# Optimization experiments

Measured on AMD Instinct MI355X. Metric: run time of the kernel, lower is better.

The kernel has to match this reference:

```python
import jax, jax.numpy as jnp
import numpy as np

B, S, F_IN, F_OUT, K = 4, 4096, 64, 64, 32


def setup_inputs() -> dict:
    key = jax.random.key(0)
    k1, k2, k3 = jax.random.split(key, 3)
    X = jax.random.normal(k1, (B, S, F_IN), dtype=jnp.float32)
    M = jax.random.normal(k2, (B, S, K), dtype=jnp.float32)
    # xavier_uniform for weight: bound = sqrt(6/(fan_in+fan_out))
    bound = float(np.sqrt(6.0 / (F_IN + F_OUT)))
    weight = jax.random.uniform(k3, (F_IN, F_OUT), dtype=jnp.float32,
                                minval=-bound, maxval=bound)
    bias = jnp.zeros((F_OUT,), dtype=jnp.float32)
    return {"X": X, "M": M, "weight": weight, "bias": bias}


def reference(X, M, weight, bias):
    # similarity = softmax(relu(M M^T), axis=-1)  -> [B, S, S]
    sim_raw = jnp.einsum('bsk,btk->bst', M, M)
    sim = jax.nn.softmax(jax.nn.relu(sim_raw), axis=-1)
    # X W  -> [B, S, F_OUT]
    Xw = jnp.einsum('bsf,fo->bso', X, weight)
    # mode='add': (I + A) Xw = Xw + A @ Xw  (identity matmul folded)
    Z = Xw + jnp.einsum('bst,bto->bso', sim, Xw)
    Z = Z + bias
    # dropout is identity at inference (eval mode)
    return Z
```

## Files before the change

kernel.cpp:

```cpp
#include <hip/hip_runtime.h>
#include <cstdint>

#define BATCH  4
#define SLEN   4096
#define FDIM   64
#define KDIM   32
#define KSPLIT 8
#define CHUNK  (SLEN / KSPLIT)

typedef __attribute__((ext_vector_type(8))) short bf16x8;
typedef __attribute__((ext_vector_type(4))) float f32x4;

static __device__ __forceinline__ short f2bf(float f) {
    union { float f; unsigned u; } v; v.f = f;
    unsigned r = v.u + 0x7fffu + ((v.u >> 16) & 1u);
    return (short)(r >> 16);
}
static __device__ __forceinline__ float bf2f(short s) {
    union { unsigned u; float f; } v;
    v.u = ((unsigned)(unsigned short)s) << 16;
    return v.f;
}
static __device__ __forceinline__ unsigned pack2bf(float a, float b) {
    union { float f; unsigned u; } x, y; x.f = a; y.f = b;
    unsigned ra = x.u + 0x7fffu + ((x.u >> 16) & 1u);
    unsigned rb = y.u + 0x7fffu + ((y.u >> 16) & 1u);
    return __builtin_amdgcn_perm(rb, ra, 0x07060302u);
}

__global__ __launch_bounds__(256) void prep(const float4* __restrict__ M4,
                                            ushort4* __restrict__ H4,
                                            ushort4* __restrict__ L4,
                                            const float* __restrict__ X,
                                            const float4* __restrict__ W4,
                                            float4* __restrict__ V4,
                                            short* __restrict__ Vt) {
    const int blk = blockIdx.y * gridDim.x + blockIdx.x;
#pragma unroll
    for (int r = 0; r < 2; ++r) {
        int i = (blk * 2 + r) * 256 + threadIdx.x;
        float4 m = M4[i];
        ushort4 h, l;
        h.x = (unsigned short)f2bf(m.x); l.x = (unsigned short)f2bf(m.x - bf2f((short)h.x));
        h.y = (unsigned short)f2bf(m.y); l.y = (unsigned short)f2bf(m.y - bf2f((short)h.y));
        h.z = (unsigned short)f2bf(m.z); l.z = (unsigned short)f2bf(m.z - bf2f((short)h.z));
        h.w = (unsigned short)f2bf(m.w); l.w = (unsigned short)f2bf(m.w - bf2f((short)h.w));
        H4[i] = h; L4[i] = l;
    }
    __shared__ float t[64][65];
    const int b  = blockIdx.y;
    const int s0 = blockIdx.x * 64;
    const int o4 = threadIdx.x & 15;
    const int rq = threadIdx.x >> 4;
#pragma unroll
    for (int half = 0; half < 4; ++half) {
        int r = half * 16 + rq;
        const float* __restrict__ xr = X + ((size_t)b * SLEN + s0 + r) * FDIM;
        float4 acc = make_float4(0.f, 0.f, 0.f, 0.f);
#pragma unroll
        for (int f = 0; f < FDIM; ++f) {
            float4 w = W4[f * 16 + o4];
            float  x = xr[f];
            acc.x = fmaf(x, w.x, acc.x);
            acc.y = fmaf(x, w.y, acc.y);
            acc.z = fmaf(x, w.z, acc.z);
            acc.w = fmaf(x, w.w, acc.w);
        }
        V4[((size_t)b * SLEN + s0 + r) * 16 + o4] = acc;
        t[r][o4 * 4 + 0] = acc.x;
        t[r][o4 * 4 + 1] = acc.y;
        t[r][o4 * 4 + 2] = acc.z;
        t[r][o4 * 4 + 3] = acc.w;
    }
    __syncthreads();
    const int c0 = threadIdx.x & 63;
    const int r0 = threadIdx.x >> 6;
    const int pc = (c0 & 32) | (((c0 >> 2) & 3) << 3) | (((c0 >> 4) & 1) << 2)
                 | (c0 & 3);
#pragma unroll
    for (int i = 0; i < 16; ++i) {
        int f = r0 + i * 4;
        Vt[((size_t)b * FDIM + f) * SLEN + s0 + pc] = f2bf(t[c0][f]);
    }
}

__global__ __launch_bounds__(256) void attn_mfma(const short* __restrict__ Mhi,
                                                 const short* __restrict__ Mlo,
                                                 const short* __restrict__ Vt,
                                                 float* __restrict__ accP,
                                                 float* __restrict__ lP) {
    const int bid  = blockIdx.x;
    const int slab = (bid & 7) + 8 * (bid >> 8);
    const int qblk = (bid >> 3) & 31;
    const int b    = slab >> 3;
    const int ks   = slab & 7;

    const int tid  = threadIdx.x;
    const int wave = tid >> 6;
    const int lane = tid & 63;
    const int col  = lane & 15;
    const int quad = lane >> 4;
    const int qbase = qblk * 128 + wave * 32;
    const int k0    = ks * CHUNK;

    const short* __restrict__ Mbh = Mhi + (size_t)b * SLEN * KDIM;
    const short* __restrict__ Mbl = Mlo + (size_t)b * SLEN * KDIM;
    const short* __restrict__ Vb  = Vt  + (size_t)b * FDIM * SLEN;

    __shared__ short khi[2][64 * 40];
    __shared__ short klo[2][64 * 40];
    __shared__ short vsh[2][2][64 * 40];

    bf16x8 Qh[2], Ql[2];
#pragma unroll
    for (int tq = 0; tq < 2; ++tq) {
        int qo = (qbase + tq * 16 + col) * KDIM + quad * 8;
        Qh[tq] = *(const bf16x8*)(Mbh + qo);
        Ql[tq] = *(const bf16x8*)(Mbl + qo);
    }

    f32x4 accf[2][4];
#pragma unroll
    for (int tq = 0; tq < 2; ++tq)
#pragma unroll
        for (int fg = 0; fg < 4; ++fg) accf[tq][fg] = (f32x4){0.f, 0.f, 0.f, 0.f};
    float lacc[2] = {0.f, 0.f};

    const int srow  = tid >> 2;
    const int spart = tid & 3;

    {
        bf16x8 rkh = *(const bf16x8*)(Mbh + (k0 + srow) * KDIM + spart * 8);
        bf16x8 rkl = *(const bf16x8*)(Mbl + (k0 + srow) * KDIM + spart * 8);
        bf16x8 rv0 = *(const bf16x8*)(Vb + (size_t)srow * SLEN + k0 + spart * 8);
        bf16x8 rv1 = *(const bf16x8*)(Vb + (size_t)srow * SLEN + k0 + 32 + spart * 8);
        *(bf16x8*)(khi[0]    + srow * 40 + spart * 8) = rkh;
        *(bf16x8*)(klo[0]    + srow * 40 + spart * 8) = rkl;
        *(bf16x8*)(vsh[0][0] + srow * 40 + spart * 8) = rv0;
        *(bf16x8*)(vsh[0][1] + srow * 40 + spart * 8) = rv1;
    }
    __syncthreads();

    int p = 0;
#pragma unroll 1
    for (int kt = k0; kt < k0 + CHUNK; kt += 64) {
        const int ktn  = kt + 64;
        const bool more = ktn < k0 + CHUNK;
        bf16x8 nkh, nkl, nv0, nv1;
        if (more) {
            nkh = *(const bf16x8*)(Mbh + (ktn + srow) * KDIM + spart * 8);
            nkl = *(const bf16x8*)(Mbl + (ktn + srow) * KDIM + spart * 8);
            nv0 = *(const bf16x8*)(Vb + (size_t)srow * SLEN + ktn + spart * 8);
            nv1 = *(const bf16x8*)(Vb + (size_t)srow * SLEN + ktn + 32 + spart * 8);
        }

        const short* __restrict__ KH = khi[p];
        const short* __restrict__ KL = klo[p];
        bf16x8 Kh[4], Kl[4];
#pragma unroll
        for (int t = 0; t < 4; ++t) {
            Kh[t] = *(const bf16x8*)(KH + (t * 16 + col) * 40 + quad * 8);
            Kl[t] = *(const bf16x8*)(KL + (t * 16 + col) * 40 + quad * 8);
        }
        bf16x8 Vv[4][2];
#pragma unroll
        for (int fg = 0; fg < 4; ++fg)
#pragma unroll
            for (int h = 0; h < 2; ++h)
                Vv[fg][h] = *(const bf16x8*)(vsh[p][h]
                                             + (fg * 16 + col) * 40 + quad * 8);

#pragma unroll
        for (int tq = 0; tq < 2; ++tq) {
            f32x4 z = (f32x4){0.f, 0.f, 0.f, 0.f};
            f32x4 c[4];
#pragma unroll
            for (int t = 0; t < 4; ++t) {
                c[t] = __builtin_amdgcn_mfma_f32_16x16x32_bf16(Kh[t], Ql[tq], z, 0, 0, 0);
                c[t] = __builtin_amdgcn_mfma_f32_16x16x32_bf16(Kl[t], Qh[tq], c[t], 0, 0, 0);
                c[t] = __builtin_amdgcn_mfma_f32_16x16x32_bf16(Kh[t], Qh[tq], c[t], 0, 0, 0);
            }
#pragma unroll
            for (int g = 0; g < 2; ++g) {
                float e0 = __expf(fmaxf(c[2 * g][0], 0.f));
                float e1 = __expf(fmaxf(c[2 * g][1], 0.f));
                float e2 = __expf(fmaxf(c[2 * g][2], 0.f));
                float e3 = __expf(fmaxf(c[2 * g][3], 0.f));
                float e4 = __expf(fmaxf(c[2 * g + 1][0], 0.f));
                float e5 = __expf(fmaxf(c[2 * g + 1][1], 0.f));
                float e6 = __expf(fmaxf(c[2 * g + 1][2], 0.f));
                float e7 = __expf(fmaxf(c[2 * g + 1][3], 0.f));
                lacc[tq] += ((e0 + e1) + (e2 + e3)) + ((e4 + e5) + (e6 + e7));

                union { unsigned u[4]; bf16x8 v; } pa;
                pa.u[0] = pack2bf(e0, e1);
                pa.u[1] = pack2bf(e2, e3);
                pa.u[2] = pack2bf(e4, e5);
                pa.u[3] = pack2bf(e6, e7);
#pragma unroll
                for (int fg = 0; fg < 4; ++fg)
                    accf[tq][fg] = __builtin_amdgcn_mfma_f32_16x16x32_bf16(
                        pa.v, Vv[fg][g], accf[tq][fg], 0, 0, 0);
            }
        }

        if (more) {
            *(bf16x8*)(khi[p ^ 1]    + srow * 40 + spart * 8) = nkh;
            *(bf16x8*)(klo[p ^ 1]    + srow * 40 + spart * 8) = nkl;
            *(bf16x8*)(vsh[p ^ 1][0] + srow * 40 + spart * 8) = nv0;
            *(bf16x8*)(vsh[p ^ 1][1] + srow * 40 + spart * 8) = nv1;
        }
        __syncthreads();
        p ^= 1;
    }

#pragma unroll
    for (int tq = 0; tq < 2; ++tq) {
#pragma unroll
        for (int j = 0; j < 4; ++j) {
            int q = qbase + tq * 16 + quad * 4 + j;
            size_t base = ((size_t)b * SLEN + q) * KSPLIT + ks;
            float* __restrict__ op = accP + base * FDIM;
#pragma unroll
            for (int fg = 0; fg < 4; ++fg)
                op[fg * 16 + col] = accf[tq][fg][j];
        }
        float lv = lacc[tq];
        lv += __shfl_xor(lv, 16);
        lv += __shfl_xor(lv, 32);
        if (quad == 0) {
            int q = qbase + tq * 16 + col;
            lP[((size_t)b * SLEN + q) * KSPLIT + ks] = lv;
        }
    }
}

__global__ __launch_bounds__(256) void combine_kernel(const float4* __restrict__ V4,
                                                      const float4* __restrict__ accP4,
                                                      const float* __restrict__ lP,
                                                      const float4* __restrict__ bias4,
                                                      float4* __restrict__ out4) {
    int i  = blockIdx.x * 256 + threadIdx.x;
    int o4 = i & 15;
    int row = i >> 4;
    float nx = 0.f, ny = 0.f, nz = 0.f, nw = 0.f, den = 0.f;
#pragma unroll
    for (int k = 0; k < KSPLIT; ++k) {
        float4 a = accP4[((size_t)row * KSPLIT + k) * 16 + o4];
        nx += a.x; ny += a.y; nz += a.z; nw += a.w;
        den += lP[(size_t)row * KSPLIT + k];
    }
    float r = 1.f / den;
    float4 v = V4[i];
    float4 bb = bias4[o4];
    float4 o;
    o.x = v.x + nx * r + bb.x;
    o.y = v.y + ny * r + bb.y;
    o.z = v.z + nz * r + bb.z;
    o.w = v.w + nw * r + bb.w;
    out4[i] = o;
}

extern "C" void kernel_launch(void* const* d_in, const int* in_sizes, int n_in,
                              void* d_out, int out_size, void* d_ws, size_t ws_size,
                              hipStream_t stream) {
    const float* X    = (const float*)d_in[0];
    const float* M    = (const float*)d_in[1];
    const float* W    = (const float*)d_in[2];
    const float* bias = (const float*)d_in[3];
    float* out = (float*)d_out;

    const size_t vElems = (size_t)BATCH * SLEN * FDIM;
    const size_t mElems = (size_t)BATCH * SLEN * KDIM;
    const size_t rows   = (size_t)BATCH * SLEN;

    float* Vf   = (float*)d_ws;
    float* accP = Vf + vElems;
    float* lP   = accP + vElems * KSPLIT;
    short* Mhi  = (short*)(lP + rows * KSPLIT);
    short* Mlo  = Mhi + mElems;
    short* Vt   = Mlo + mElems;

    prep<<<dim3(SLEN / 64, BATCH), 256, 0, stream>>>(
        (const float4*)M, (ushort4*)Mhi, (ushort4*)Mlo,
        X, (const float4*)W, (float4*)Vf, Vt);

    attn_mfma<<<dim3((SLEN / 128) * BATCH * KSPLIT), 256, 0, stream>>>(
        Mhi, Mlo, Vt, accP, lP);

    combine_kernel<<<(int)(vElems / 1024), 256, 0, stream>>>(
        (const float4*)Vf, (const float4*)accP, lP, (const float4*)bias,
        (float4*)out);
}
```

Baseline: 124.2 us.

## Double queries per wave, pre-scale Q by log2e, and drop LDS double buffering

Each wave now handles 64 queries instead of 32, so every K/V tile staged in LDS is reused across twice as many query rows, and the grid is halved. The query copy of M is pre-multiplied by log2(e) in the prep kernel, so the softmax exponent can use the native exp2 instead of __expf. The PV product is reordered so each V fragment is read from LDS once and applied to all four query tiles. LDS double buffering is replaced by a single buffer with two barriers per tile, with occupancy set through launch_bounds(256,2). This trades fewer blocks, more registers and the loss of load/compute overlap for better reuse and cheaper exponentials.

```diff
diff --git a/kernel.cpp b/kernel.cpp
--- a/kernel.cpp
+++ b/kernel.cpp
@@ -31,21 +31,29 @@
 __global__ __launch_bounds__(256) void prep(const float4* __restrict__ M4,
                                             ushort4* __restrict__ H4,
                                             ushort4* __restrict__ L4,
+                                            ushort4* __restrict__ QH4,
+                                            ushort4* __restrict__ QL4,
                                             const float* __restrict__ X,
                                             const float4* __restrict__ W4,
                                             float4* __restrict__ V4,
                                             short* __restrict__ Vt) {
     const int blk = blockIdx.y * gridDim.x + blockIdx.x;
+    const float LOG2E = 1.4426950408889634f;
 #pragma unroll
     for (int r = 0; r < 2; ++r) {
         int i = (blk * 2 + r) * 256 + threadIdx.x;
         float4 m = M4[i];
-        ushort4 h, l;
+        ushort4 h, l, sh, sl;
         h.x = (unsigned short)f2bf(m.x); l.x = (unsigned short)f2bf(m.x - bf2f((short)h.x));
         h.y = (unsigned short)f2bf(m.y); l.y = (unsigned short)f2bf(m.y - bf2f((short)h.y));
         h.z = (unsigned short)f2bf(m.z); l.z = (unsigned short)f2bf(m.z - bf2f((short)h.z));
         h.w = (unsigned short)f2bf(m.w); l.w = (unsigned short)f2bf(m.w - bf2f((short)h.w));
-        H4[i] = h; L4[i] = l;
+        float sx = m.x * LOG2E, sy = m.y * LOG2E, sz = m.z * LOG2E, sw = m.w * LOG2E;
+        sh.x = (unsigned short)f2bf(sx); sl.x = (unsigned short)f2bf(sx - bf2f((short)sh.x));
+        sh.y = (unsigned short)f2bf(sy); sl.y = (unsigned short)f2bf(sy - bf2f((short)sh.y));
+        sh.z = (unsigned short)f2bf(sz); sl.z = (unsigned short)f2bf(sz - bf2f((short)sh.z));
+        sh.w = (unsigned short)f2bf(sw); sl.w = (unsigned short)f2bf(sw - bf2f((short)sh.w));
+        H4[i] = h; L4[i] = l; QH4[i] = sh; QL4[i] = sl;
     }
     __shared__ float t[64][65];
     const int b  = blockIdx.y;
@@ -84,94 +92,79 @@
     }
 }
 
-__global__ __launch_bounds__(256) void attn_mfma(const short* __restrict__ Mhi,
-                                                 const short* __restrict__ Mlo,
-                                                 const short* __restrict__ Vt,
-                                                 float* __restrict__ accP,
-                                                 float* __restrict__ lP) {
+__global__ __launch_bounds__(256, 2) void attn_mfma(const short* __restrict__ Mhi,
+                                                    const short* __restrict__ Mlo,
+                                                    const short* __restrict__ Qhi,
+                                                    const short* __restrict__ Qlo,
+                                                    const short* __restrict__ Vt,
+                                                    float* __restrict__ accP,
+                                                    float* __restrict__ lP) {
     const int bid  = blockIdx.x;
-    const int slab = (bid & 7) + 8 * (bid >> 8);
-    const int qblk = (bid >> 3) & 31;
-    const int b    = slab >> 3;
-    const int ks   = slab & 7;
+    const int xcd  = bid & 7;
+    const int slot = bid >> 3;
+    const int g    = xcd + 8 * (slot >> 4);
+    const int qblk = slot & 15;
+    const int b    = g >> 3;
+    const int ks   = g & 7;
 
     const int tid  = threadIdx.x;
     const int wave = tid >> 6;
     const int lane = tid & 63;
     const int col  = lane & 15;
     const int quad = lane >> 4;
-    const int qbase = qblk * 128 + wave * 32;
+    const int qbase = qblk * 256 + wave * 64;
     const int k0    = ks * CHUNK;
 
     const short* __restrict__ Mbh = Mhi + (size_t)b * SLEN * KDIM;
     const short* __restrict__ Mbl = Mlo + (size_t)b * SLEN * KDIM;
+    const short* __restrict__ Qbh = Qhi + (size_t)b * SLEN * KDIM;
+    const short* __restrict__ Qbl = Qlo + (size_t)b * SLEN * KDIM;
     const short* __restrict__ Vb  = Vt  + (size_t)b * FDIM * SLEN;
 
-    __shared__ short khi[2][64 * 40];
-    __shared__ short klo[2][64 * 40];
-    __shared__ short vsh[2][2][64 * 40];
-
-    bf16x8 Qh[2], Ql[2];
-#pragma unroll
-    for (int tq = 0; tq < 2; ++tq) {
+    __shared__ short khi[64 * 40];
+    __shared__ short klo[64 * 40];
+    __shared__ short vsh[2][64 * 40];
+
+    bf16x8 Qh[4], Ql[4];
+#pragma unroll
+    for (int tq = 0; tq < 4; ++tq) {
         int qo = (qbase + tq * 16 + col) * KDIM + quad * 8;
-        Qh[tq] = *(const bf16x8*)(Mbh + qo);
-        Ql[tq] = *(const bf16x8*)(Mbl + qo);
-    }
-
-    f32x4 accf[2][4];
-#pragma unroll
-    for (int tq = 0; tq < 2; ++tq)
+        Qh[tq] = *(const bf16x8*)(Qbh + qo);
+        Ql[tq] = *(const bf16x8*)(Qbl + qo);
+    }
+
+    f32x4 accf[4][4];
+#pragma unroll
+    for (int tq = 0; tq < 4; ++tq)
 #pragma unroll
         for (int fg = 0; fg < 4; ++fg) accf[tq][fg] = (f32x4){0.f, 0.f, 0.f, 0.f};
-    float lacc[2] = {0.f, 0.f};
+    float lacc[4] = {0.f, 0.f, 0.f, 0.f};
 
     const int srow  = tid >> 2;
     const int spart = tid & 3;
 
-    {
-        bf16x8 rkh = *(const bf16x8*)(Mbh + (k0 + srow) * KDIM + spart * 8);
-        bf16x8 rkl = *(const bf16x8*)(Mbl + (k0 + srow) * KDIM + spart * 8);
-        bf16x8 rv0 = *(const bf16x8*)(Vb + (size_t)srow * SLEN + k0 + spart * 8);
-        bf16x8 rv1 = *(const bf16x8*)(Vb + (size_t)srow * SLEN + k0 + 32 + spart * 8);
-        *(bf16x8*)(khi[0]    + srow * 40 + spart * 8) = rkh;
-        *(bf16x8*)(klo[0]    + srow * 40 + spart * 8) = rkl;
-        *(bf16x8*)(vsh[0][0] + srow * 40 + spart * 8) = rv0;
-        *(bf16x8*)(vsh[0][1] + srow * 40 + spart * 8) = rv1;
-    }
-    __syncthreads();
-
-    int p = 0;
 #pragma unroll 1
     for (int kt = k0; kt < k0 + CHUNK; kt += 64) {
-        const int ktn  = kt + 64;
-        const bool more = ktn < k0 + CHUNK;
-        bf16x8 nkh, nkl, nv0, nv1;
-        if (more) {
-            nkh = *(const bf16x8*)(Mbh + (ktn + srow) * KDIM + spart * 8);
-            nkl = *(const bf16x8*)(Mbl + (ktn + srow) * KDIM + spart * 8);
-            nv0 = *(const bf16x8*)(Vb + (size_t)srow * SLEN + ktn + spart * 8);
-            nv1 = *(const bf16x8*)(Vb + (size_t)srow * SLEN + ktn + 32 + spart * 8);
-        }
-
-        const short* __restrict__ KH = khi[p];
-        const short* __restrict__ KL = klo[p];
+        bf16x8 rkh = *(const bf16x8*)(Mbh + (kt + srow) * KDIM + spart * 8);
+        bf16x8 rkl = *(const bf16x8*)(Mbl + (kt + srow) * KDIM + spart * 8);
+        bf16x8 rv0 = *(const bf16x8*)(Vb + (size_t)srow * SLEN + kt + spart * 8);
+        bf16x8 rv1 = *(const bf16x8*)(Vb + (size_t)srow * SLEN + kt + 32 + spart * 8);
+        __syncthreads();
+        *(bf16x8*)(khi    + srow * 40 + spart * 8) = rkh;
+        *(bf16x8*)(klo    + srow * 40 + spart * 8) = rkl;
+        *(bf16x8*)(vsh[0] + srow * 40 + spart * 8) = rv0;
+        *(bf16x8*)(vsh[1] + srow * 40 + spart * 8) = rv1;
+        __syncthreads();
+
         bf16x8 Kh[4], Kl[4];
 #pragma unroll
         for (int t = 0; t < 4; ++t) {
-            Kh[t] = *(const bf16x8*)(KH + (t * 16 + col) * 40 + quad * 8);
-            Kl[t] = *(const bf16x8*)(KL + (t * 16 + col) * 40 + quad * 8);
-        }
-        bf16x8 Vv[4][2];
-#pragma unroll
-        for (int fg = 0; fg < 4; ++fg)
-#pragma unroll
-            for (int h = 0; h < 2; ++h)
-                Vv[fg][h] = *(const bf16x8*)(vsh[p][h]
-                                             + (fg * 16 + col) * 40 + quad * 8);
-
-#pragma unroll
-        for (int tq = 0; tq < 2; ++tq) {
+            Kh[t] = *(const bf16x8*)(khi + (t * 16 + col) * 40 + quad * 8);
+            Kl[t] = *(const bf16x8*)(klo + (t * 16 + col) * 40 + quad * 8);
+        }
+        bf16x8 paf[4][2];
+#pragma unroll
+        for (int tq = 0; tq < 4; ++tq) {
             f32x4 z = (f32x4){0.f, 0.f, 0.f, 0.f};
             f32x4 c[4];
 #pragma unroll
@@ -181,41 +174,41 @@
                 c[t] = __builtin_amdgcn_mfma_f32_16x16x32_bf16(Kh[t], Qh[tq], c[t], 0, 0, 0);
             }
 #pragma unroll
-            for (int g = 0; g < 2; ++g) {
-                float e0 = __expf(fmaxf(c[2 * g][0], 0.f));
-                float e1 = __expf(fmaxf(c[2 * g][1], 0.f));
-                float e2 = __expf(fmaxf(c[2 * g][2], 0.f));
-                float e3 = __expf(fmaxf(c[2 * g][3], 0.f));
-                float e4 = __expf(fmaxf(c[2 * g + 1][0], 0.f));
-                float e5 = __expf(fmaxf(c[2 * g + 1][1], 0.f));
-                float e6 = __expf(fmaxf(c[2 * g + 1][2], 0.f));
-                float e7 = __expf(fmaxf(c[2 * g + 1][3], 0.f));
+            for (int gr = 0; gr < 2; ++gr) {
+                float e0 = __builtin_amdgcn_exp2f(fmaxf(c[2 * gr][0], 0.f));
+                float e1 = __builtin_amdgcn_exp2f(fmaxf(c[2 * gr][1], 0.f));
+                float e2 = __builtin_amdgcn_exp2f(fmaxf(c[2 * gr][2], 0.f));
+                float e3 = __builtin_amdgcn_exp2f(fmaxf(c[2 * gr][3], 0.f));
+                float e4 = __builtin_amdgcn_exp2f(fmaxf(c[2 * gr + 1][0], 0.f));
+                float e5 = __builtin_amdgcn_exp2f(fmaxf(c[2 * gr + 1][1], 0.f));
+                float e6 = __builtin_amdgcn_exp2f(fmaxf(c[2 * gr + 1][2], 0.f));
+                float e7 = __builtin_amdgcn_exp2f(fmaxf(c[2 * gr + 1][3], 0.f));
                 lacc[tq] += ((e0 + e1) + (e2 + e3)) + ((e4 + e5) + (e6 + e7));
-
                 union { unsigned u[4]; bf16x8 v; } pa;
                 pa.u[0] = pack2bf(e0, e1);
                 pa.u[1] = pack2bf(e2, e3);
                 pa.u[2] = pack2bf(e4, e5);
                 pa.u[3] = pack2bf(e6, e7);
-#pragma unroll
-                for (int fg = 0; fg < 4; ++fg)
+                paf[tq][gr] = pa.v;
+            }
+        }
+
+#pragma unroll
+        for (int gr = 0; gr < 2; ++gr) {
+#pragma unroll
+            for (int fg = 0; fg < 4; ++fg) {
+                bf16x8 Vv = *(const bf16x8*)(vsh[gr] + (fg * 16 + col) * 40
+                                             + quad * 8);
+#pragma unroll
+                for (int tq = 0; tq < 4; ++tq)
                     accf[tq][fg] = __builtin_amdgcn_mfma_f32_16x16x32_bf16(
-                        pa.v, Vv[fg][g], accf[tq][fg], 0, 0, 0);
+                        paf[tq][gr], Vv, accf[tq][fg], 0, 0, 0);
             }
         }
-
-        if (more) {
-            *(bf16x8*)(khi[p ^ 1]    + srow * 40 + spart * 8) = nkh;
-            *(bf16x8*)(klo[p ^ 1]    + srow * 40 + spart * 8) = nkl;
-            *(bf16x8*)(vsh[p ^ 1][0] + srow * 40 + spart * 8) = nv0;
-            *(bf16x8*)(vsh[p ^ 1][1] + srow * 40 + spart * 8) = nv1;
-        }
-        __syncthreads();
-        p ^= 1;
-    }
-
-#pragma unroll
-    for (int tq = 0; tq < 2; ++tq) {
+    }
+
+#pragma unroll
+    for (int tq = 0; tq < 4; ++tq) {
 #pragma unroll
         for (int j = 0; j < 4; ++j) {
             int q = qbase + tq * 16 + quad * 4 + j;
@@ -279,14 +272,17 @@
     float* lP   = accP + vElems * KSPLIT;
     short* Mhi  = (short*)(lP + rows * KSPLIT);
     short* Mlo  = Mhi + mElems;
-    short* Vt   = Mlo + mElems;
+    short* Qhi  = Mlo + mElems;
+    short* Qlo  = Qhi + mElems;
+    short* Vt   = Qlo + mElems;
 
     prep<<<dim3(SLEN / 64, BATCH), 256, 0, stream>>>(
         (const float4*)M, (ushort4*)Mhi, (ushort4*)Mlo,
+        (ushort4*)Qhi, (ushort4*)Qlo,
         X, (const float4*)W, (float4*)Vf, Vt);
 
-    attn_mfma<<<dim3((SLEN / 128) * BATCH * KSPLIT), 256, 0, stream>>>(
-        Mhi, Mlo, Vt, accP, lP);
+    attn_mfma<<<dim3((SLEN / 256) * BATCH * KSPLIT), 256, 0, stream>>>(
+        Mhi, Mlo, Qhi, Qlo, Vt, accP, lP);
 
     combine_kernel<<<(int)(vElems / 1024), 256, 0, stream>>>(
         (const float4*)Vf, (const float4*)accP, lP, (const float4*)bias,
```

Result: no change. 124.0 us (-0.2%).
